# Performance work log

Measured on AMD Instinct MI355X. Metric: run time of the kernel, lower is better.

The kernel has to match this reference:

```python
import jax, jax.numpy as jnp
import numpy as np
from jax import lax

K = 3  # neighbors, as in torch_geometric.nn.knn_interpolate default
EPS = 1e-16


def knn_interpolate(x, pos_x, pos_y):
    """Interpolate features x defined at pos_x onto query points pos_y.
    x: [Ns, F], pos_x: [Ns, 3], pos_y: [Nq, 3] -> [Nq, F].
    Inverse squared-distance weighting over K nearest neighbors."""
    # squared distances via the |y|^2 + |x|^2 - 2 y.x expansion (no [Nq,Ns,3] temp)
    d2 = (jnp.sum(pos_y * pos_y, -1, keepdims=True)
          + jnp.sum(pos_x * pos_x, -1)[None, :]
          - 2.0 * pos_y @ pos_x.T)                      # [Nq, Ns]
    neg_d2, idx = lax.top_k(-d2, K)                      # [Nq, K]
    w = 1.0 / jnp.clip(-neg_d2, EPS)                     # inverse squared distance
    w = w / jnp.sum(w, -1, keepdims=True)
    return jnp.einsum('qk,qkf->qf', w, x[idx])           # gather + weighted reduce


def mlp(x, W1, b1, W2, b2, W3, b3):
    x = jax.nn.relu(x @ W1 + b1)
    x = jax.nn.relu(x @ W2 + b2)
    return x @ W3 + b3


def setup_inputs() -> dict:
    key = jax.random.key(0)
    ks = jax.random.split(key, 16)
    Nh, Nl, H, O = 16384, 4096, 256, 3
    s = lambda fan: 1.0 / np.sqrt(fan)
    return {
        'emb1':  jax.random.normal(ks[0], (Nh, H), jnp.float32),
        'l_y1':  jax.random.normal(ks[1], (Nl, O), jnp.float32),
        'l_pos1': jax.random.uniform(ks[2], (Nl, 3), jnp.float32),
        'h_pos1': jax.random.uniform(ks[3], (Nh, 3), jnp.float32),
        'emb2':  jax.random.normal(ks[4], (Nh, H), jnp.float32),
        'l_y2':  jax.random.normal(ks[5], (Nl, O), jnp.float32),
        'l_pos2': jax.random.uniform(ks[6], (Nl, 3), jnp.float32),
        'h_pos2': jax.random.uniform(ks[7], (Nh, 3), jnp.float32),
        'W1': jax.random.uniform(ks[8], (H, H), jnp.float32, -s(H), s(H)),
        'b1': jax.random.uniform(ks[9], (H,), jnp.float32, -s(H), s(H)),
        'W2': jax.random.uniform(ks[10], (H, H), jnp.float32, -s(H), s(H)),
        'b2': jax.random.uniform(ks[11], (H,), jnp.float32, -s(H), s(H)),
        'W3': jax.random.uniform(ks[12], (H, O), jnp.float32, -s(H), s(H)),
        'b3': jax.random.uniform(ks[13], (O,), jnp.float32, -s(H), s(H)),
    }


def reference(emb1, l_y1, l_pos1, h_pos1, emb2, l_y2, l_pos2, h_pos2,
              W1, b1, W2, b2, W3, b3):
    x = mlp(emb1 - knn_interpolate(emb2, h_pos2, h_pos1), W1, b1, W2, b2, W3, b3)
    # residual=True branch
    res = knn_interpolate(l_y1 - knn_interpolate(l_y2, l_pos2, l_pos1), l_pos1, h_pos1)
    return x + res
```

## Files before the change

kernel.cpp:

```cpp
#include <hip/hip_runtime.h>
#include <math.h>

#define BIGF 3.0e38f

typedef short  s16x8 __attribute__((ext_vector_type(8)));
typedef float  f32x4 __attribute__((ext_vector_type(4)));

__device__ __forceinline__ unsigned short f2bf(float x) {
  unsigned int b = __float_as_uint(x);
  unsigned int r = b + 0x7FFFu + ((b >> 16) & 1u);
  return (unsigned short)(r >> 16);
}
__device__ __forceinline__ float bf2f(unsigned short h) {
  return __uint_as_float(((unsigned int)h) << 16);
}


__device__ __forceinline__ int cell_clamp(float v, int G) {
  int c = (int)(v * (float)G);
  return min(G - 1, max(0, c));
}

__device__ __forceinline__ void ins3(float d, int id,
                                     float& d0, float& d1, float& d2,
                                     int& i0, int& i1, int& i2) {
  bool l0 = (d < d0) || (d == d0 && id < i0);
  bool l1 = (d < d1) || (d == d1 && id < i1);
  bool l2 = (d < d2) || (d == d2 && id < i2);
  float nd0 = l0 ? d  : d0;  int ni0 = l0 ? id : i0;
  float nd1 = l0 ? d0 : (l1 ? d  : d1);
  int   ni1 = l0 ? i0 : (l1 ? id : i1);
  float nd2 = l1 ? d1 : (l2 ? d  : d2);
  int   ni2 = l1 ? i1 : (l2 ? id : i2);
  d0 = nd0; d1 = nd1; d2 = nd2; i0 = ni0; i1 = ni1; i2 = ni2;
}

__device__ __forceinline__ void scan_shell(
    int R, int sl, int G, int cx, int cy, int cz,
    const int* __restrict__ offs, const float4* __restrict__ spts,
    const int* __restrict__ sidx,
    float qx, float qy, float qz, float sy,
    float& d0, float& d1, float& d2v, int& i0, int& i1, int& i2)
{
  #pragma clang fp contract(off)
  #define SCANP()                                                             \
    { int j = js;                                                             \
      if (j < je) {                                                           \
        float4 sc = spts[j]; int idc = sidx[j];                               \
        for (++j; ; ++j) {                                                    \
          bool more = (j < je);                                               \
          float4 sn; int idn;                                                 \
          if (more) { sn = spts[j]; idn = sidx[j]; }                          \
          float p0 = qx * sc.x, p1 = qy * sc.y, p2 = qz * sc.z;               \
          float dt = (p0 + p1) + p2;                                          \
          float S  = sy + sc.w;                                               \
          float dd = S - 2.0f * dt;                                           \
          ins3(dd, idc, d0, d1, d2v, i0, i1, i2);                             \
          if (!more) break;                                                   \
          sc = sn; idc = idn;                                                 \
        }                                                                     \
      } }

  if (R == 1) {
    if (sl < 9) {
      int dy = sl % 3 - 1, dz = sl / 3 - 1;
      int yy = cy + dy, zz = cz + dz;
      if (yy >= 0 && yy < G && zz >= 0 && zz < G) {
        int xs = max(cx - 1, 0), xe = min(cx + 1, G - 1);
        int base = (zz * G + yy) * G;
        int js = offs[base + xs], je = offs[base + xe + 1];
        SCANP()
      }
    }
  } else {
    const int twoR1 = 2 * R + 1, inner = 2 * R - 1;
    const int nfz = 2 * twoR1;
    const int nfull = nfz + 2 * inner;
    const int half = inner * inner;
    const int nitems = nfull + 2 * half;
    for (int m = sl; m < nitems; m += 16) {
      int dy, dz, js, je;
      if (m < nfull) {
        if (m < nfz) { dz = (m < twoR1) ? -R : R; dy = (m % twoR1) - R; }
        else { int u = m - nfz; dy = (u < inner) ? -R : R; dz = (u % inner) - (R - 1); }
        int yy = cy + dy, zz = cz + dz;
        if (yy < 0 || yy >= G || zz < 0 || zz >= G) continue;
        int xs = max(cx - R, 0), xe = min(cx + R, G - 1);
        int base = (zz * G + yy) * G;
        js = offs[base + xs]; je = offs[base + xe + 1];
      } else {
        int u = m - nfull;
        int xc = (u < half) ? (cx - R) : (cx + R);
        int r2 = (u < half) ? u : u - half;
        dy = r2 % inner - (R - 1); dz = r2 / inner - (R - 1);
        int yy = cy + dy, zz = cz + dz;
        if (xc < 0 || xc >= G || yy < 0 || yy >= G || zz < 0 || zz >= G) continue;
        int c = (zz * G + yy) * G + xc;
        js = offs[c]; je = offs[c + 1];
      }
      SCANP()
    }
  }
  #undef SCANP
}

#define MERGE16(E0, E1, E2, J0, J1, J2)                                       \
  { _Pragma("unroll")                                                         \
    for (int msk = 1; msk < 16; msk <<= 1) {                                  \
      float o0 = __shfl_xor(E0, msk), o1 = __shfl_xor(E1, msk), o2 = __shfl_xor(E2, msk); \
      int   p0 = __shfl_xor(J0, msk), p1 = __shfl_xor(J1, msk), p2 = __shfl_xor(J2, msk); \
      ins3(o0, p0, E0, E1, E2, J0, J1, J2);                                   \
      ins3(o1, p1, E0, E1, E2, J0, J1, J2);                                   \
      ins3(o2, p2, E0, E1, E2, J0, J1, J2);                                   \
    } }

__device__ void knn_bt_body(
    int bid,
    const float4* __restrict__ qspts, const int* __restrict__ qsidx, int Nq,
    int GA, const int* __restrict__ offsA, const float4* __restrict__ sptsA, const int* __restrict__ sidxA,
    int GB, const int* __restrict__ offsB, const float4* __restrict__ sptsB, const int* __restrict__ sidxB,
    float* __restrict__ wC_out, int* __restrict__ iC_out,
    const float* __restrict__ emb1, const float* __restrict__ emb2,
    unsigned short* __restrict__ t_hi, unsigned short* __restrict__ t_lo)
{
  const int sl = threadIdx.x & 15;
  const int qs = bid * 16 + (threadIdx.x >> 4);
  if (qs >= Nq) return;

  float4 qv = qspts[qs];
  const float qx = qv.x, qy = qv.y, qz = qv.z;
  const float sy = qv.w;
  const int qorig = qsidx[qs];
  const float csA = 1.0f / (float)GA, csB = 1.0f / (float)GB;
  const int cxA = cell_clamp(qx, GA), cyA = cell_clamp(qy, GA), czA = cell_clamp(qz, GA);
  const int cxB = cell_clamp(qx, GB), cyB = cell_clamp(qy, GB), czB = cell_clamp(qz, GB);

  float a0 = BIGF, a1 = BIGF, a2 = BIGF;  int ia0 = -1, ia1 = -1, ia2 = -1;
  float b0 = BIGF, b1 = BIGF, b2 = BIGF;  int ib0 = -1, ib1 = -1, ib2 = -1;
  float eA0 = BIGF, eA1 = BIGF, eA2 = BIGF; int jA0 = -1, jA1 = -1, jA2 = -1;
  float eB0 = BIGF, eB1 = BIGF, eB2 = BIGF; int jB0 = -1, jB1 = -1, jB2 = -1;
  bool doneA = false, doneB = false;

  const int Gmax = max(GA, GB);
  for (int R = 1; R <= Gmax; ++R) {
    if (!doneA && R <= GA)
      scan_shell(R, sl, GA, cxA, cyA, czA, offsA, sptsA, sidxA,
                 qx, qy, qz, sy, a0, a1, a2, ia0, ia1, ia2);
    if (!doneB && R <= GB)
      scan_shell(R, sl, GB, cxB, cyB, czB, offsB, sptsB, sidxB,
                 qx, qy, qz, sy, b0, b1, b2, ib0, ib1, ib2);
    if (!doneA && R <= GA) {
      eA0 = a0; eA1 = a1; eA2 = a2; jA0 = ia0; jA1 = ia1; jA2 = ia2;
      MERGE16(eA0, eA1, eA2, jA0, jA1, jA2)
      float bnd = (float)R * csA;
      doneA = (eA2 <= bnd * bnd - 1e-6f) || (R >= GA);
    }
    if (!doneB && R <= GB) {
      eB0 = b0; eB1 = b1; eB2 = b2; jB0 = ib0; jB1 = ib1; jB2 = ib2;
      MERGE16(eB0, eB1, eB2, jB0, jB1, jB2)
      float bnd = (float)R * csB;
      doneB = (eB2 <= bnd * bnd - 1e-6f) || (R >= GB);
    }
    if (__all(doneA && doneB)) break;
  }

  if (sl == 0) {
    float w0 = 1.0f / fmaxf(eB0, 1e-16f);
    float w1 = 1.0f / fmaxf(eB1, 1e-16f);
    float w2 = 1.0f / fmaxf(eB2, 1e-16f);
    float inv = 1.0f / (w0 + w1 + w2);
    wC_out[(size_t)qorig * 3 + 0] = w0 * inv;
    wC_out[(size_t)qorig * 3 + 1] = w1 * inv;
    wC_out[(size_t)qorig * 3 + 2] = w2 * inv;
    iC_out[(size_t)qorig * 3 + 0] = jB0;
    iC_out[(size_t)qorig * 3 + 1] = jB1;
    iC_out[(size_t)qorig * 3 + 2] = jB2;
  }

  {
    float w0 = 1.0f / fmaxf(eA0, 1e-16f);
    float w1 = 1.0f / fmaxf(eA1, 1e-16f);
    float w2 = 1.0f / fmaxf(eA2, 1e-16f);
    float inv = 1.0f / (w0 + w1 + w2);
    w0 *= inv; w1 *= inv; w2 *= inv;
    const float4* e1 = (const float4*)emb1;
    const float4* e2 = (const float4*)emb2;
    #pragma unroll
    for (int k = 0; k < 4; ++k) {
      int c4 = sl + 16 * k;
      float4 a  = e1[(size_t)qorig * 64 + c4];
      float4 f0 = e2[(size_t)jA0 * 64 + c4];
      float4 f1 = e2[(size_t)jA1 * 64 + c4];
      float4 f2 = e2[(size_t)jA2 * 64 + c4];
      float4 r;
      r.x = a.x - (w0 * f0.x + w1 * f1.x + w2 * f2.x);
      r.y = a.y - (w0 * f0.y + w1 * f1.y + w2 * f2.y);
      r.z = a.z - (w0 * f0.z + w1 * f1.z + w2 * f2.z);
      r.w = a.w - (w0 * f0.w + w1 * f1.w + w2 * f2.w);
      ushort4 h, l;
      h.x = f2bf(r.x); l.x = f2bf(r.x - bf2f(h.x));
      h.y = f2bf(r.y); l.y = f2bf(r.y - bf2f(h.y));
      h.z = f2bf(r.z); l.z = f2bf(r.z - bf2f(h.z));
      h.w = f2bf(r.w); l.w = f2bf(r.w - bf2f(h.w));
      size_t o = (size_t)qorig * 256 + (size_t)c4 * 4;
      *(ushort4*)&t_hi[o] = h;
      *(ushort4*)&t_lo[o] = l;
    }
  }
}

__device__ void knn_single_body(
    int bid,
    const float4* __restrict__ qspts, const int* __restrict__ qsidx, int Nq, int G,
    const int* __restrict__ offs, const float4* __restrict__ spts, const int* __restrict__ sidx,
    const float* __restrict__ base3, const float* __restrict__ feat3,
    float* __restrict__ out3)
{
  #pragma clang fp contract(off)
  const int sl = threadIdx.x & 15;
  const int qs = bid * 16 + (threadIdx.x >> 4);
  if (qs >= Nq) return;

  float4 qv = qspts[qs];
  const float qx = qv.x, qy = qv.y, qz = qv.z;
  const float sy = qv.w;
  const int qorig = qsidx[qs];
  const float cs = 1.0f / (float)G;
  const int cx = cell_clamp(qx, G), cy = cell_clamp(qy, G), cz = cell_clamp(qz, G);

  float d0 = BIGF, d1 = BIGF, d2v = BIGF;
  int i0 = -1, i1 = -1, i2 = -1;
  float e0 = BIGF, e1 = BIGF, e2 = BIGF;
  int j0 = -1, j1 = -1, j2 = -1;
  bool done = false;

  for (int R = 1; R <= G; ++R) {
    if (!done) {
      scan_shell(R, sl, G, cx, cy, cz, offs, spts, sidx,
                 qx, qy, qz, sy, d0, d1, d2v, i0, i1, i2);
      e0 = d0; e1 = d1; e2 = d2v; j0 = i0; j1 = i1; j2 = i2;
      MERGE16(e0, e1, e2, j0, j1, j2)
      float bnd = (float)R * cs;
      done = (e2 <= bnd * bnd - 1e-6f) || (R >= G);
    }
    if (__all(done)) break;
  }

  if (sl == 0) {
    float w0 = 1.0f / fmaxf(e0, 1e-16f);
    float w1 = 1.0f / fmaxf(e1, 1e-16f);
    float w2 = 1.0f / fmaxf(e2, 1e-16f);
    float inv = 1.0f / (w0 + w1 + w2);
    w0 *= inv; w1 *= inv; w2 *= inv;
    #pragma unroll
    for (int f = 0; f < 3; ++f) {
      float v = w0 * feat3[(size_t)j0 * 3 + f]
              + w1 * feat3[(size_t)j1 * 3 + f]
              + w2 * feat3[(size_t)j2 * 3 + f];
      out3[(size_t)qorig * 3 + f] = base3[(size_t)qorig * 3 + f] - v;
    }
  }
}

__device__ void res_gather_body(
    int bid, const float* __restrict__ wC, const int* __restrict__ idxC,
    const float* __restrict__ diff, float* __restrict__ res, int Nq)
{
  int q = bid * 256 + threadIdx.x;
  if (q >= Nq) return;
  float w0 = wC[(size_t)q * 3 + 0], w1 = wC[(size_t)q * 3 + 1], w2 = wC[(size_t)q * 3 + 2];
  int i0 = idxC[(size_t)q * 3 + 0], i1 = idxC[(size_t)q * 3 + 1], i2 = idxC[(size_t)q * 3 + 2];
  #pragma unroll
  for (int f = 0; f < 3; ++f) {
    res[(size_t)q * 3 + f] = w0 * diff[(size_t)i0 * 3 + f]
                           + w1 * diff[(size_t)i1 * 3 + f]
                           + w2 * diff[(size_t)i2 * 3 + f];
  }
}

__global__ __launch_bounds__(256) void knn_bt_kernel(
    const float4* qspts, const int* qsidx, int Nh,
    int G1, const int* offs1, const float4* spts1, const int* sidx1,
    int G2, const int* offs3, const float4* spts3, const int* sidx3,
    float* wC, int* idxC,
    const float* emb1, const float* emb2,
    unsigned short* t_hi, unsigned short* t_lo,
    int Nl, const int* offs2, const float4* spts2, const int* sidx2,
    const float* l_y1, const float* l_y2, float* diff)
{
  int g = blockIdx.x / 5, r = blockIdx.x % 5;
  if (r < 4)
    knn_bt_body(g * 4 + r, qspts, qsidx, Nh,
                G1, offs1, spts1, sidx1,
                G2, offs3, spts3, sidx3, wC, idxC,
                emb1, emb2, t_hi, t_lo);
  else
    knn_single_body(g, spts3, sidx3, Nl, G2, offs2, spts2, sidx2,
                    l_y1, l_y2, diff);
}

__global__ __launch_bounds__(256) void zero_kernel(int* __restrict__ p, int n) {
  int i = blockIdx.x * 256 + threadIdx.x;
  if (i < n) p[i] = 0;
}

__global__ __launch_bounds__(256) void count_split_kernel(
    const float* __restrict__ p1, int n1, int g1, int* __restrict__ c1,
    const float* __restrict__ p2, int n2, int g2, int* __restrict__ c2,
    const float* __restrict__ p3, int n3, int g3, int* __restrict__ c3,
    const float* __restrict__ p4, int n4, int g4, int* __restrict__ c4,
    const float* __restrict__ W1, unsigned short* __restrict__ h1T, unsigned short* __restrict__ l1T,
    const float* __restrict__ W2, unsigned short* __restrict__ h2T, unsigned short* __restrict__ l2T)
{
  int b = blockIdx.x;
  if (b >= 160) {
    int sb = b - 160;
    const float* W = (sb < 256) ? W1 : W2;
    unsigned short* hiT = (sb < 256) ? h1T : h2T;
    unsigned short* loT = (sb < 256) ? l1T : l2T;
    int id = (sb & 255) * 256 + threadIdx.x;
    int k = id >> 8, n = id & 255;
    float x = W[id];
    unsigned short h = f2bf(x);
    unsigned short l = f2bf(x - bf2f(h));
    hiT[n * 256 + k] = h;
    loT[n * 256 + k] = l;
    return;
  }
  const float* p; int n, G; int* cnt; int i;
  if (b < 64)       { p = p1; n = n1; G = g1; cnt = c1; i = b * 256 + threadIdx.x; }
  else if (b < 80)  { p = p2; n = n2; G = g2; cnt = c2; i = (b - 64) * 256 + threadIdx.x; }
  else if (b < 96)  { p = p3; n = n3; G = g3; cnt = c3; i = (b - 80) * 256 + threadIdx.x; }
  else              { p = p4; n = n4; G = g4; cnt = c4; i = (b - 96) * 256 + threadIdx.x; }
  if (i >= n) return;
  int cx = cell_clamp(p[3 * i],     G);
  int cy = cell_clamp(p[3 * i + 1], G);
  int cz = cell_clamp(p[3 * i + 2], G);
  atomicAdd(&cnt[(cz * G + cy) * G + cx], 1);
}

__global__ __launch_bounds__(256) void prefix4_kernel(
    const int* __restrict__ c1, int* __restrict__ o1, int* __restrict__ u1, int m1,
    const int* __restrict__ c2, int* __restrict__ o2, int* __restrict__ u2, int m2,
    const int* __restrict__ c3, int* __restrict__ o3, int* __restrict__ u3, int m3,
    const int* __restrict__ c4, int* __restrict__ o4, int* __restrict__ u4, int m4)
{
  const int* cnt; int* offs; int* cur; int M;
  if (blockIdx.x == 0)      { cnt = c1; offs = o1; cur = u1; M = m1; }
  else if (blockIdx.x == 1) { cnt = c2; offs = o2; cur = u2; M = m2; }
  else if (blockIdx.x == 2) { cnt = c3; offs = o3; cur = u3; M = m3; }
  else                      { cnt = c4; offs = o4; cur = u4; M = m4; }
  __shared__ int ps[256];
  const int tid = threadIdx.x;
  const int per = (M + 255) >> 8;
  const int base = tid * per;
  int s = 0;
  for (int j = 0; j < per; ++j) if (base + j < M) s += cnt[base + j];
  ps[tid] = s;
  __syncthreads();
  for (int off = 1; off < 256; off <<= 1) {
    int v = (tid >= off) ? ps[tid - off] : 0;
    __syncthreads();
    ps[tid] += v;
    __syncthreads();
  }
  int run = (tid > 0) ? ps[tid - 1] : 0;
  for (int j = 0; j < per; ++j) {
    if (base + j < M) {
      offs[base + j] = run; cur[base + j] = run;
      run += cnt[base + j];
    }
  }
  if (tid == 255) offs[M] = run;
}

__global__ __launch_bounds__(256) void scatter4_kernel(
    const float* __restrict__ p1, int n1, int g1, int* __restrict__ u1, float4* __restrict__ s1, int* __restrict__ x1,
    const float* __restrict__ p2, int n2, int g2, int* __restrict__ u2, float4* __restrict__ s2, int* __restrict__ x2,
    const float* __restrict__ p3, int n3, int g3, int* __restrict__ u3, float4* __restrict__ s3, int* __restrict__ x3,
    const float* __restrict__ p4, int n4, int g4, int* __restrict__ u4, float4* __restrict__ s4, int* __restrict__ x4)
{
  #pragma clang fp contract(off)
  int b = blockIdx.x;
  const float* p; int n, G; int* cur; float4* spts; int* sidx; int i;
  if (b < 64)       { p = p1; n = n1; G = g1; cur = u1; spts = s1; sidx = x1; i = b * 256 + threadIdx.x; }
  else if (b < 80)  { p = p2; n = n2; G = g2; cur = u2; spts = s2; sidx = x2; i = (b - 64) * 256 + threadIdx.x; }
  else if (b < 96)  { p = p3; n = n3; G = g3; cur = u3; spts = s3; sidx = x3; i = (b - 80) * 256 + threadIdx.x; }
  else              { p = p4; n = n4; G = g4; cur = u4; spts = s4; sidx = x4; i = (b - 96) * 256 + threadIdx.x; }
  if (i >= n) return;
  float x = p[3 * i], y = p[3 * i + 1], z = p[3 * i + 2];
  int cx = cell_clamp(x, G), cy = cell_clamp(y, G), cz = cell_clamp(z, G);
  int c = (cz * G + cy) * G + cx;
  int pos = atomicAdd(&cur[c], 1);
  float sx = (x * x + y * y) + z * z;
  spts[pos] = make_float4(x, y, z, sx);
  sidx[pos] = i;
}

__global__ __launch_bounds__(256) void mfma_gemm_kernel(
    const unsigned short* __restrict__ A_hi, const unsigned short* __restrict__ A_lo,
    const unsigned short* __restrict__ BT_hi, const unsigned short* __restrict__ BT_lo,
    const float* __restrict__ bias,
    float* __restrict__ outf,
    unsigned short* __restrict__ out_hi, unsigned short* __restrict__ out_lo,
    int relu, int split_out, int ngemm,
    const float* __restrict__ wC, const int* __restrict__ idxC,
    const float* __restrict__ diff, float* __restrict__ resout, int NqG)
{
  __shared__ unsigned short Bs_hi[64][132];
  __shared__ unsigned short Bs_lo[64][132];
  const int t = threadIdx.x;
  const int d = blockIdx.x;
  if (d >= ngemm) {
    res_gather_body(d - ngemm, wC, idxC, diff, resout, NqG);
    return;
  }
  const int xcd = d & 7, slot = d >> 3;
  const int lin = xcd * (ngemm >> 3) + slot;
  const int row0 = (lin >> 2) * 64;
  const int col0 = (lin & 3) * 64;

  const int l = t & 63, w = t >> 6;
  const int lr = l & 15;
  const int lk = (l >> 4) << 3;
  const unsigned short* arh = A_hi + (size_t)(row0 + w * 16 + lr) * 256;
  const unsigned short* arl = A_lo + (size_t)(row0 + w * 16 + lr) * 256;

  const int sc = t >> 2;
  const int sk = (t & 3) << 5;

  f32x4 acc0 = {0.f,0.f,0.f,0.f}, acc1 = {0.f,0.f,0.f,0.f};
  f32x4 acc2 = {0.f,0.f,0.f,0.f}, acc3 = {0.f,0.f,0.f,0.f};

  #define KSTEP(CT, ACC)                                                      \
    { s16x8 bh = *(const s16x8*)&Bs_hi[CT * 16 + lr][kc + lk];                \
      s16x8 bl = *(const s16x8*)&Bs_lo[CT * 16 + lr][kc + lk];                \
      ACC = __builtin_amdgcn_mfma_f32_16x16x32_bf16(ah, bh, ACC, 0, 0, 0);    \
      ACC = __builtin_amdgcn_mfma_f32_16x16x32_bf16(al, bh, ACC, 0, 0, 0);    \
      ACC = __builtin_amdgcn_mfma_f32_16x16x32_bf16(ah, bl, ACC, 0, 0, 0); }

  for (int half = 0; half < 2; ++half) {
    if (half) __syncthreads();
    {
      const int4* sh = (const int4*)&BT_hi[(size_t)(col0 + sc) * 256 + half * 128 + sk];
      const int4* slo = (const int4*)&BT_lo[(size_t)(col0 + sc) * 256 + half * 128 + sk];
      int4* dh = (int4*)&Bs_hi[sc][sk];
      int4* dl = (int4*)&Bs_lo[sc][sk];
      #pragma unroll
      for (int i = 0; i < 4; ++i) { dh[i] = sh[i]; dl[i] = slo[i]; }
    }
    __syncthreads();
    const int kbase = half * 128;
    #pragma unroll
    for (int kc = 0; kc < 128; kc += 32) {
      s16x8 ah = *(const s16x8*)&arh[kbase + kc + lk];
      s16x8 al = *(const s16x8*)&arl[kbase + kc + lk];
      KSTEP(0, acc0)
      KSTEP(1, acc1)
      KSTEP(2, acc2)
      KSTEP(3, acc3)
    }
  }
  #undef KSTEP

  const int orow = row0 + w * 16 + ((l >> 4) << 2);
  #define EPILOG(CT, ACC)                                                     \
    { int col = col0 + CT * 16 + lr;                                          \
      float bb = bias[col];                                                   \
      _Pragma("unroll")                                                       \
      for (int r = 0; r < 4; ++r) {                                           \
        float v = ACC[r] + bb;                                                \
        if (relu) v = fmaxf(v, 0.0f);                                         \
        size_t o = (size_t)(orow + r) * 256 + col;                            \
        if (split_out) {                                                      \
          unsigned short hh = f2bf(v);                                        \
          out_hi[o] = hh; out_lo[o] = f2bf(v - bf2f(hh));                     \
        } else {                                                              \
          outf[o] = v;                                                        \
        }                                                                     \
      } }
  EPILOG(0, acc0)
  EPILOG(1, acc1)
  EPILOG(2, acc2)
  EPILOG(3, acc3)
  #undef EPILOG
}

__global__ __launch_bounds__(256) void final_kernel(
    const float* __restrict__ h2, const float* __restrict__ W3,
    const float* __restrict__ b3, const float* __restrict__ res,
    float* __restrict__ out, int M)
{
  __shared__ float sW3[768];
  const int tid = threadIdx.x;
  for (int i = tid; i < 768; i += 256) sW3[i] = W3[i];
  __syncthreads();

  const int wave = tid >> 6, lane = tid & 63;
  const int r = blockIdx.x * 4 + wave;
  if (r >= M) return;

  float4 h = ((const float4*)h2)[(size_t)r * 64 + lane];
  const int c = lane * 4;
  float a0 = h.x * sW3[(c + 0) * 3 + 0] + h.y * sW3[(c + 1) * 3 + 0]
           + h.z * sW3[(c + 2) * 3 + 0] + h.w * sW3[(c + 3) * 3 + 0];
  float a1 = h.x * sW3[(c + 0) * 3 + 1] + h.y * sW3[(c + 1) * 3 + 1]
           + h.z * sW3[(c + 2) * 3 + 1] + h.w * sW3[(c + 3) * 3 + 1];
  float a2 = h.x * sW3[(c + 0) * 3 + 2] + h.y * sW3[(c + 1) * 3 + 2]
           + h.z * sW3[(c + 2) * 3 + 2] + h.w * sW3[(c + 3) * 3 + 2];

  #pragma unroll
  for (int off = 32; off; off >>= 1) {
    a0 += __shfl_xor(a0, off);
    a1 += __shfl_xor(a1, off);
    a2 += __shfl_xor(a2, off);
  }
  if (lane == 0) {
    out[(size_t)r * 3 + 0] = a0 + b3[0] + res[(size_t)r * 3 + 0];
    out[(size_t)r * 3 + 1] = a1 + b3[1] + res[(size_t)r * 3 + 1];
    out[(size_t)r * 3 + 2] = a2 + b3[2] + res[(size_t)r * 3 + 2];
  }
}

extern "C" void kernel_launch(void* const* d_in, const int* in_sizes, int n_in,
                              void* d_out, int out_size, void* d_ws, size_t ws_size,
                              hipStream_t stream) {
  (void)in_sizes; (void)n_in; (void)out_size; (void)ws_size;
  const float* emb1   = (const float*)d_in[0];
  const float* l_y1   = (const float*)d_in[1];
  const float* l_pos1 = (const float*)d_in[2];
  const float* h_pos1 = (const float*)d_in[3];
  const float* emb2   = (const float*)d_in[4];
  const float* l_y2   = (const float*)d_in[5];
  const float* l_pos2 = (const float*)d_in[6];
  const float* h_pos2 = (const float*)d_in[7];
  const float* W1     = (const float*)d_in[8];
  const float* b1     = (const float*)d_in[9];
  const float* W2     = (const float*)d_in[10];
  const float* b2     = (const float*)d_in[11];
  const float* W3     = (const float*)d_in[12];
  const float* b3     = (const float*)d_in[13];
  float* out = (float*)d_out;

  const int Nh = 16384, Nl = 4096, H = 256;
  const int G1 = 16, G2 = 10;
  const int M1 = G1 * G1 * G1, M2 = G2 * G2 * G2;

  char* wsp = (char*)d_ws;
  size_t off = 0;
  auto alloc = [&](size_t bytes) -> void* {
    void* p = wsp + off;
    off += (bytes + 255) & ~(size_t)255;
    return p;
  };
  int*            idxC   = (int*)           alloc((size_t)Nh * 3 * 4);
  float*          wC     = (float*)         alloc((size_t)Nh * 3 * 4);
  unsigned short* t_hi   = (unsigned short*)alloc((size_t)Nh * H * 2);
  unsigned short* t_lo   = (unsigned short*)alloc((size_t)Nh * H * 2);
  unsigned short* h1_hi  = (unsigned short*)alloc((size_t)Nh * H * 2);
  unsigned short* h1_lo  = (unsigned short*)alloc((size_t)Nh * H * 2);
  float*          h2     = (float*)t_hi;
  unsigned short* w1t_hi = (unsigned short*)alloc((size_t)H * H * 2);
  unsigned short* w1t_lo = (unsigned short*)alloc((size_t)H * H * 2);
  unsigned short* w2t_hi = (unsigned short*)alloc((size_t)H * H * 2);
  unsigned short* w2t_lo = (unsigned short*)alloc((size_t)H * H * 2);
  float*          diff   = (float*)         alloc((size_t)Nl * 3 * 4);
  float*          res    = (float*)         alloc((size_t)Nh * 3 * 4);
  int*            cnts   = (int*)           alloc((size_t)(M1 + M2 + M2 + M1) * 4);
  int* cnt1 = cnts, *cnt2 = cnts + M1, *cnt3 = cnts + M1 + M2, *cnt4 = cnts + M1 + 2 * M2;
  int*            offs1  = (int*)           alloc((size_t)(M1 + 1) * 4);
  int*            cur1   = (int*)           alloc((size_t)M1 * 4);
  int*            offs2  = (int*)           alloc((size_t)(M2 + 1) * 4);
  int*            cur2   = (int*)           alloc((size_t)M2 * 4);
  int*            offs3  = (int*)           alloc((size_t)(M2 + 1) * 4);
  int*            cur3   = (int*)           alloc((size_t)M2 * 4);
  int*            offs4  = (int*)           alloc((size_t)(M1 + 1) * 4);
  int*            cur4   = (int*)           alloc((size_t)M1 * 4);
  float4*         spts1  = (float4*)        alloc((size_t)Nh * 16);
  int*            sidx1  = (int*)           alloc((size_t)Nh * 4);
  float4*         spts2  = (float4*)        alloc((size_t)Nl * 16);
  int*            sidx2  = (int*)           alloc((size_t)Nl * 4);
  float4*         spts3  = (float4*)        alloc((size_t)Nl * 16);
  int*            sidx3  = (int*)           alloc((size_t)Nl * 4);
  float4*         qspts  = (float4*)        alloc((size_t)Nh * 16);
  int*            qsidx  = (int*)           alloc((size_t)Nh * 4);

  const int ncnt = M1 + M2 + M2 + M1;
  zero_kernel<<<(ncnt + 255) / 256, 256, 0, stream>>>(cnts, ncnt);
  count_split_kernel<<<672, 256, 0, stream>>>(
      h_pos2, Nh, G1, cnt1,  l_pos2, Nl, G2, cnt2,
      l_pos1, Nl, G2, cnt3,  h_pos1, Nh, G1, cnt4,
      W1, w1t_hi, w1t_lo, W2, w2t_hi, w2t_lo);
  prefix4_kernel<<<4, 256, 0, stream>>>(
      cnt1, offs1, cur1, M1,  cnt2, offs2, cur2, M2,
      cnt3, offs3, cur3, M2,  cnt4, offs4, cur4, M1);
  scatter4_kernel<<<160, 256, 0, stream>>>(
      h_pos2, Nh, G1, cur1, spts1, sidx1,
      l_pos2, Nl, G2, cur2, spts2, sidx2,
      l_pos1, Nl, G2, cur3, spts3, sidx3,
      h_pos1, Nh, G1, cur4, qspts, qsidx);

  knn_bt_kernel<<<1280, 256, 0, stream>>>(
      qspts, qsidx, Nh,
      G1, offs1, spts1, sidx1,
      G2, offs3, spts3, sidx3, wC, idxC,
      emb1, emb2, t_hi, t_lo,
      Nl, offs2, spts2, sidx2, l_y1, l_y2, diff);

  mfma_gemm_kernel<<<1024 + 64, 256, 0, stream>>>(
      t_hi, t_lo, w1t_hi, w1t_lo, b1, nullptr, h1_hi, h1_lo, 1, 1, 1024,
      wC, idxC, diff, res, Nh);
  mfma_gemm_kernel<<<1024, 256, 0, stream>>>(
      h1_hi, h1_lo, w2t_hi, w2t_lo, b2, h2, nullptr, nullptr, 1, 0, 1024,
      nullptr, nullptr, nullptr, nullptr, 0);

  final_kernel<<<Nh / 4, 256, 0, stream>>>(h2, W3, b3, res, out, Nh);
}
```

Measured before the change: 119.5 us.

## Split fused dual KNN search into separate blocks and unroll cell scan by four

The combined body that searched two grids (emb2 positions and l_pos1 positions) for each high-res query is split into two independent block types, each running a shared single-grid search helper. The kernel grid grows from 1280 to 2304 blocks, with 4 emb-interpolation, 4 weight-producing and 1 low-res block per group. The point-scan loop replaces the software-prefetched single-point loop with a four-way unrolled loop plus a remainder. The aim is to spread work over more waves, cut per-thread register pressure, and add memory-level parallelism. In exchange, query loading and cell setup are repeated for the two searches.

```diff
diff --git a/kernel.cpp b/kernel.cpp
--- a/kernel.cpp
+++ b/kernel.cpp
@@ -43,22 +43,26 @@
     float& d0, float& d1, float& d2v, int& i0, int& i1, int& i2)
 {
   #pragma clang fp contract(off)
+  #define DIST_INS(SV, IDV)                                                   \
+    { float p0 = qx * SV.x, p1 = qy * SV.y, p2 = qz * SV.z;                   \
+      float dt = (p0 + p1) + p2;                                              \
+      float S  = sy + SV.w;                                                   \
+      float dd = S - 2.0f * dt;                                               \
+      ins3(dd, IDV, d0, d1, d2v, i0, i1, i2); }
+
   #define SCANP()                                                             \
     { int j = js;                                                             \
-      if (j < je) {                                                           \
-        float4 sc = spts[j]; int idc = sidx[j];                               \
-        for (++j; ; ++j) {                                                    \
-          bool more = (j < je);                                               \
-          float4 sn; int idn;                                                 \
-          if (more) { sn = spts[j]; idn = sidx[j]; }                          \
-          float p0 = qx * sc.x, p1 = qy * sc.y, p2 = qz * sc.z;               \
-          float dt = (p0 + p1) + p2;                                          \
-          float S  = sy + sc.w;                                               \
-          float dd = S - 2.0f * dt;                                           \
-          ins3(dd, idc, d0, d1, d2v, i0, i1, i2);                             \
-          if (!more) break;                                                   \
-          sc = sn; idc = idn;                                                 \
-        }                                                                     \
+      for (; j + 4 <= je; j += 4) {                                           \
+        float4 s0 = spts[j],     s1 = spts[j + 1];                            \
+        float4 s2 = spts[j + 2], s3 = spts[j + 3];                            \
+        int id0 = sidx[j],     id1 = sidx[j + 1];                             \
+        int id2 = sidx[j + 2], id3 = sidx[j + 3];                             \
+        DIST_INS(s0, id0) DIST_INS(s1, id1)                                   \
+        DIST_INS(s2, id2) DIST_INS(s3, id3)                                   \
+      }                                                                       \
+      for (; j < je; ++j) {                                                   \
+        float4 s = spts[j]; int id = sidx[j];                                 \
+        DIST_INS(s, id)                                                       \
       } }
 
   if (R == 1) {
@@ -102,6 +106,7 @@
     }
   }
   #undef SCANP
+  #undef DIST_INS
 }
 
 #define MERGE16(E0, E1, E2, J0, J1, J2)                                       \
@@ -114,126 +119,17 @@
       ins3(o2, p2, E0, E1, E2, J0, J1, J2);                                   \
     } }
 
-__device__ void knn_bt_body(
-    int bid,
-    const float4* __restrict__ qspts, const int* __restrict__ qsidx, int Nq,
-    int GA, const int* __restrict__ offsA, const float4* __restrict__ sptsA, const int* __restrict__ sidxA,
-    int GB, const int* __restrict__ offsB, const float4* __restrict__ sptsB, const int* __restrict__ sidxB,
-    float* __restrict__ wC_out, int* __restrict__ iC_out,
-    const float* __restrict__ emb1, const float* __restrict__ emb2,
-    unsigned short* __restrict__ t_hi, unsigned short* __restrict__ t_lo)
-{
-  const int sl = threadIdx.x & 15;
-  const int qs = bid * 16 + (threadIdx.x >> 4);
-  if (qs >= Nq) return;
-
-  float4 qv = qspts[qs];
-  const float qx = qv.x, qy = qv.y, qz = qv.z;
-  const float sy = qv.w;
-  const int qorig = qsidx[qs];
-  const float csA = 1.0f / (float)GA, csB = 1.0f / (float)GB;
-  const int cxA = cell_clamp(qx, GA), cyA = cell_clamp(qy, GA), czA = cell_clamp(qz, GA);
-  const int cxB = cell_clamp(qx, GB), cyB = cell_clamp(qy, GB), czB = cell_clamp(qz, GB);
-
-  float a0 = BIGF, a1 = BIGF, a2 = BIGF;  int ia0 = -1, ia1 = -1, ia2 = -1;
-  float b0 = BIGF, b1 = BIGF, b2 = BIGF;  int ib0 = -1, ib1 = -1, ib2 = -1;
-  float eA0 = BIGF, eA1 = BIGF, eA2 = BIGF; int jA0 = -1, jA1 = -1, jA2 = -1;
-  float eB0 = BIGF, eB1 = BIGF, eB2 = BIGF; int jB0 = -1, jB1 = -1, jB2 = -1;
-  bool doneA = false, doneB = false;
-
-  const int Gmax = max(GA, GB);
-  for (int R = 1; R <= Gmax; ++R) {
-    if (!doneA && R <= GA)
-      scan_shell(R, sl, GA, cxA, cyA, czA, offsA, sptsA, sidxA,
-                 qx, qy, qz, sy, a0, a1, a2, ia0, ia1, ia2);
-    if (!doneB && R <= GB)
-      scan_shell(R, sl, GB, cxB, cyB, czB, offsB, sptsB, sidxB,
-                 qx, qy, qz, sy, b0, b1, b2, ib0, ib1, ib2);
-    if (!doneA && R <= GA) {
-      eA0 = a0; eA1 = a1; eA2 = a2; jA0 = ia0; jA1 = ia1; jA2 = ia2;
-      MERGE16(eA0, eA1, eA2, jA0, jA1, jA2)
-      float bnd = (float)R * csA;
-      doneA = (eA2 <= bnd * bnd - 1e-6f) || (R >= GA);
-    }
-    if (!doneB && R <= GB) {
-      eB0 = b0; eB1 = b1; eB2 = b2; jB0 = ib0; jB1 = ib1; jB2 = ib2;
-      MERGE16(eB0, eB1, eB2, jB0, jB1, jB2)
-      float bnd = (float)R * csB;
-      doneB = (eB2 <= bnd * bnd - 1e-6f) || (R >= GB);
-    }
-    if (__all(doneA && doneB)) break;
-  }
-
-  if (sl == 0) {
-    float w0 = 1.0f / fmaxf(eB0, 1e-16f);
-    float w1 = 1.0f / fmaxf(eB1, 1e-16f);
-    float w2 = 1.0f / fmaxf(eB2, 1e-16f);
-    float inv = 1.0f / (w0 + w1 + w2);
-    wC_out[(size_t)qorig * 3 + 0] = w0 * inv;
-    wC_out[(size_t)qorig * 3 + 1] = w1 * inv;
-    wC_out[(size_t)qorig * 3 + 2] = w2 * inv;
-    iC_out[(size_t)qorig * 3 + 0] = jB0;
-    iC_out[(size_t)qorig * 3 + 1] = jB1;
-    iC_out[(size_t)qorig * 3 + 2] = jB2;
-  }
-
-  {
-    float w0 = 1.0f / fmaxf(eA0, 1e-16f);
-    float w1 = 1.0f / fmaxf(eA1, 1e-16f);
-    float w2 = 1.0f / fmaxf(eA2, 1e-16f);
-    float inv = 1.0f / (w0 + w1 + w2);
-    w0 *= inv; w1 *= inv; w2 *= inv;
-    const float4* e1 = (const float4*)emb1;
-    const float4* e2 = (const float4*)emb2;
-    #pragma unroll
-    for (int k = 0; k < 4; ++k) {
-      int c4 = sl + 16 * k;
-      float4 a  = e1[(size_t)qorig * 64 + c4];
-      float4 f0 = e2[(size_t)jA0 * 64 + c4];
-      float4 f1 = e2[(size_t)jA1 * 64 + c4];
-      float4 f2 = e2[(size_t)jA2 * 64 + c4];
-      float4 r;
-      r.x = a.x - (w0 * f0.x + w1 * f1.x + w2 * f2.x);
-      r.y = a.y - (w0 * f0.y + w1 * f1.y + w2 * f2.y);
-      r.z = a.z - (w0 * f0.z + w1 * f1.z + w2 * f2.z);
-      r.w = a.w - (w0 * f0.w + w1 * f1.w + w2 * f2.w);
-      ushort4 h, l;
-      h.x = f2bf(r.x); l.x = f2bf(r.x - bf2f(h.x));
-      h.y = f2bf(r.y); l.y = f2bf(r.y - bf2f(h.y));
-      h.z = f2bf(r.z); l.z = f2bf(r.z - bf2f(h.z));
-      h.w = f2bf(r.w); l.w = f2bf(r.w - bf2f(h.w));
-      size_t o = (size_t)qorig * 256 + (size_t)c4 * 4;
-      *(ushort4*)&t_hi[o] = h;
-      *(ushort4*)&t_lo[o] = l;
-    }
-  }
-}
-
-__device__ void knn_single_body(
-    int bid,
-    const float4* __restrict__ qspts, const int* __restrict__ qsidx, int Nq, int G,
-    const int* __restrict__ offs, const float4* __restrict__ spts, const int* __restrict__ sidx,
-    const float* __restrict__ base3, const float* __restrict__ feat3,
-    float* __restrict__ out3)
-{
-  #pragma clang fp contract(off)
-  const int sl = threadIdx.x & 15;
-  const int qs = bid * 16 + (threadIdx.x >> 4);
-  if (qs >= Nq) return;
-
-  float4 qv = qspts[qs];
-  const float qx = qv.x, qy = qv.y, qz = qv.z;
-  const float sy = qv.w;
-  const int qorig = qsidx[qs];
+__device__ __forceinline__ void knn_search(
+    int sl, float qx, float qy, float qz, float sy, int G,
+    const int* __restrict__ offs, const float4* __restrict__ spts,
+    const int* __restrict__ sidx,
+    float& e0, float& e1, float& e2, int& j0, int& j1, int& j2)
+{
   const float cs = 1.0f / (float)G;
   const int cx = cell_clamp(qx, G), cy = cell_clamp(qy, G), cz = cell_clamp(qz, G);
-
   float d0 = BIGF, d1 = BIGF, d2v = BIGF;
   int i0 = -1, i1 = -1, i2 = -1;
-  float e0 = BIGF, e1 = BIGF, e2 = BIGF;
-  int j0 = -1, j1 = -1, j2 = -1;
   bool done = false;
-
   for (int R = 1; R <= G; ++R) {
     if (!done) {
       scan_shell(R, sl, G, cx, cy, cz, offs, spts, sidx,
@@ -245,6 +141,101 @@
     }
     if (__all(done)) break;
   }
+}
+
+__device__ void knn0_bt_body(
+    int bid,
+    const float4* __restrict__ qspts, const int* __restrict__ qsidx, int Nq,
+    int G, const int* __restrict__ offs, const float4* __restrict__ spts, const int* __restrict__ sidx,
+    const float* __restrict__ emb1, const float* __restrict__ emb2,
+    unsigned short* __restrict__ t_hi, unsigned short* __restrict__ t_lo)
+{
+  const int sl = threadIdx.x & 15;
+  const int qs = bid * 16 + (threadIdx.x >> 4);
+  if (qs >= Nq) return;
+  float4 qv = qspts[qs];
+  const int qorig = qsidx[qs];
+
+  float e0, e1, e2; int j0, j1, j2;
+  knn_search(sl, qv.x, qv.y, qv.z, qv.w, G, offs, spts, sidx,
+             e0, e1, e2, j0, j1, j2);
+
+  float w0 = 1.0f / fmaxf(e0, 1e-16f);
+  float w1 = 1.0f / fmaxf(e1, 1e-16f);
+  float w2 = 1.0f / fmaxf(e2, 1e-16f);
+  float inv = 1.0f / (w0 + w1 + w2);
+  w0 *= inv; w1 *= inv; w2 *= inv;
+  const float4* e1p = (const float4*)emb1;
+  const float4* e2p = (const float4*)emb2;
+  #pragma unroll
+  for (int k = 0; k < 4; ++k) {
+    int c4 = sl + 16 * k;
+    float4 a  = e1p[(size_t)qorig * 64 + c4];
+    float4 f0 = e2p[(size_t)j0 * 64 + c4];
+    float4 f1 = e2p[(size_t)j1 * 64 + c4];
+    float4 f2 = e2p[(size_t)j2 * 64 + c4];
+    float4 r;
+    r.x = a.x - (w0 * f0.x + w1 * f1.x + w2 * f2.x);
+    r.y = a.y - (w0 * f0.y + w1 * f1.y + w2 * f2.y);
+    r.z = a.z - (w0 * f0.z + w1 * f1.z + w2 * f2.z);
+    r.w = a.w - (w0 * f0.w + w1 * f1.w + w2 * f2.w);
+    ushort4 h, l;
+    h.x = f2bf(r.x); l.x = f2bf(r.x - bf2f(h.x));
+    h.y = f2bf(r.y); l.y = f2bf(r.y - bf2f(h.y));
+    h.z = f2bf(r.z); l.z = f2bf(r.z - bf2f(h.z));
+    h.w = f2bf(r.w); l.w = f2bf(r.w - bf2f(h.w));
+    size_t o = (size_t)qorig * 256 + (size_t)c4 * 4;
+    *(ushort4*)&t_hi[o] = h;
+    *(ushort4*)&t_lo[o] = l;
+  }
+}
+
+__device__ void knn2_body(
+    int bid,
+    const float4* __restrict__ qspts, const int* __restrict__ qsidx, int Nq,
+    int G, const int* __restrict__ offs, const float4* __restrict__ spts, const int* __restrict__ sidx,
+    float* __restrict__ wC_out, int* __restrict__ iC_out)
+{
+  const int sl = threadIdx.x & 15;
+  const int qs = bid * 16 + (threadIdx.x >> 4);
+  if (qs >= Nq) return;
+  float4 qv = qspts[qs];
+  const int qorig = qsidx[qs];
+
+  float e0, e1, e2; int j0, j1, j2;
+  knn_search(sl, qv.x, qv.y, qv.z, qv.w, G, offs, spts, sidx,
+             e0, e1, e2, j0, j1, j2);
+
+  if (sl == 0) {
+    float w0 = 1.0f / fmaxf(e0, 1e-16f);
+    float w1 = 1.0f / fmaxf(e1, 1e-16f);
+    float w2 = 1.0f / fmaxf(e2, 1e-16f);
+    float inv = 1.0f / (w0 + w1 + w2);
+    wC_out[(size_t)qorig * 3 + 0] = w0 * inv;
+    wC_out[(size_t)qorig * 3 + 1] = w1 * inv;
+    wC_out[(size_t)qorig * 3 + 2] = w2 * inv;
+    iC_out[(size_t)qorig * 3 + 0] = j0;
+    iC_out[(size_t)qorig * 3 + 1] = j1;
+    iC_out[(size_t)qorig * 3 + 2] = j2;
+  }
+}
+
+__device__ void knn1_body(
+    int bid,
+    const float4* __restrict__ qspts, const int* __restrict__ qsidx, int Nq, int G,
+    const int* __restrict__ offs, const float4* __restrict__ spts, const int* __restrict__ sidx,
+    const float* __restrict__ base3, const float* __restrict__ feat3,
+    float* __restrict__ out3)
+{
+  const int sl = threadIdx.x & 15;
+  const int qs = bid * 16 + (threadIdx.x >> 4);
+  if (qs >= Nq) return;
+  float4 qv = qspts[qs];
+  const int qorig = qsidx[qs];
+
+  float e0, e1, e2; int j0, j1, j2;
+  knn_search(sl, qv.x, qv.y, qv.z, qv.w, G, offs, spts, sidx,
+             e0, e1, e2, j0, j1, j2);
 
   if (sl == 0) {
     float w0 = 1.0f / fmaxf(e0, 1e-16f);
@@ -278,25 +269,26 @@
   }
 }
 
-__global__ __launch_bounds__(256) void knn_bt_kernel(
+__global__ __launch_bounds__(256) void knn_all_kernel(
     const float4* qspts, const int* qsidx, int Nh,
     int G1, const int* offs1, const float4* spts1, const int* sidx1,
+    const float* emb1, const float* emb2,
+    unsigned short* t_hi, unsigned short* t_lo,
     int G2, const int* offs3, const float4* spts3, const int* sidx3,
     float* wC, int* idxC,
-    const float* emb1, const float* emb2,
-    unsigned short* t_hi, unsigned short* t_lo,
     int Nl, const int* offs2, const float4* spts2, const int* sidx2,
     const float* l_y1, const float* l_y2, float* diff)
 {
-  int g = blockIdx.x / 5, r = blockIdx.x % 5;
+  int g = blockIdx.x / 9, r = blockIdx.x % 9;
   if (r < 4)
-    knn_bt_body(g * 4 + r, qspts, qsidx, Nh,
-                G1, offs1, spts1, sidx1,
-                G2, offs3, spts3, sidx3, wC, idxC,
-                emb1, emb2, t_hi, t_lo);
+    knn0_bt_body(g * 4 + r, qspts, qsidx, Nh, G1, offs1, spts1, sidx1,
+                 emb1, emb2, t_hi, t_lo);
+  else if (r < 8)
+    knn2_body(g * 4 + (r - 4), qspts, qsidx, Nh, G2, offs3, spts3, sidx3,
+              wC, idxC);
   else
-    knn_single_body(g, spts3, sidx3, Nl, G2, offs2, spts2, sidx2,
-                    l_y1, l_y2, diff);
+    knn1_body(g, spts3, sidx3, Nl, G2, offs2, spts2, sidx2,
+              l_y1, l_y2, diff);
 }
 
 __global__ __launch_bounds__(256) void zero_kernel(int* __restrict__ p, int n) {
@@ -600,11 +592,10 @@
       l_pos1, Nl, G2, cur3, spts3, sidx3,
       h_pos1, Nh, G1, cur4, qspts, qsidx);
 
-  knn_bt_kernel<<<1280, 256, 0, stream>>>(
+  knn_all_kernel<<<2304, 256, 0, stream>>>(
       qspts, qsidx, Nh,
-      G1, offs1, spts1, sidx1,
+      G1, offs1, spts1, sidx1, emb1, emb2, t_hi, t_lo,
       G2, offs3, spts3, sidx3, wC, idxC,
-      emb1, emb2, t_hi, t_lo,
       Nl, offs2, spts2, sidx2, l_y1, l_y2, diff);
 
   mfma_gemm_kernel<<<1024 + 64, 256, 0, stream>>>(
```

Result: faster. 109.0 us (-8.8%).
